# Optimization experiments

Measured on AMD Instinct MI355X. Metric: run time of the kernel, lower is better.

The kernel has to match this reference:

```python
import jax, jax.numpy as jnp
import numpy as np
from jax import lax


def setup_inputs() -> dict:
    key = jax.random.key(0)
    k1, k2, k3, k4, k5 = jax.random.split(key, 5)
    B, Cin, Cout, H, W, K, S = 16, 256, 256, 128, 128, 3, 512
    x = jax.random.normal(k1, (B, Cin, H, W), dtype=jnp.float32)
    style = jax.random.normal(k2, (B, S), dtype=jnp.float32)
    # parameters (kaiming-ish scales)
    conv_w = jax.random.normal(k3, (Cout, Cin, K, K), dtype=jnp.float32) * (1.0 / np.sqrt(Cin * K * K))
    fc_w = jax.random.normal(k4, (Cout, S), dtype=jnp.float32) * (1.0 / np.sqrt(S))
    fc_b = jax.random.normal(k5, (Cout,), dtype=jnp.float32) * 0.01
    return {"x": x, "style": style, "conv_w": conv_w, "fc_w": fc_w, "fc_b": fc_b}


def reference(x, style, conv_w, fc_w, fc_b):
    # style_fc: (B, S) @ (S, Cout) + b -> per-sample per-output-channel scale
    s = style @ fc_w.T + fc_b  # (B, Cout)
    # Modulating W[o] by s[b,o] on the output-channel axis commutes with the
    # convolution, so the per-sample loop is a single conv + channel scale.
    # (Original uses F.conv2d with bias=None, so conv bias is never applied.)
    y = lax.conv_general_dilated(
        x, conv_w,
        window_strides=(1, 1),
        padding=[(1, 1), (1, 1)],
        dimension_numbers=("NCHW", "OIHW", "NCHW"),
    )  # (B, Cout, H, W)
    return y * s[:, :, None, None]
```

## Files before the change

### kernel.cpp

```cpp
#include <hip/hip_runtime.h>
#include <stdint.h>

typedef __attribute__((ext_vector_type(8))) short bf16x8;
typedef __attribute__((ext_vector_type(8))) unsigned short u16x8;
typedef __attribute__((ext_vector_type(4))) float f32x4;

#define NB   16
#define CIN  256
#define COUT 256
#define HH   128
#define WW   128
#define SDIM 512

#define BK 64
#define KPAD 72
#define NCOL 130

#define B_BYTES (3 * NCOL * KPAD * 2)
#define S_BYTES (COUT * 4)
#define LDS_BYTES (B_BYTES + S_BYTES)

__device__ __forceinline__ unsigned short f2bf(float f) {
    unsigned int u = __float_as_uint(f);
    u += 0x7fff + ((u >> 16) & 1);
    return (unsigned short)(u >> 16);
}

__global__ void style_fc_kernel(const float* __restrict__ style,
                                const float* __restrict__ fc_w,
                                const float* __restrict__ fc_b,
                                float* __restrict__ s_out) {
    const int b = blockIdx.x;
    const int co = threadIdx.x;
    const f32x4* st = (const f32x4*)(style + b * SDIM);
    const f32x4* w  = (const f32x4*)(fc_w + co * SDIM);
    float acc = fc_b[co];
    #pragma unroll 4
    for (int k = 0; k < SDIM / 4; ++k) {
        f32x4 a = st[k], c = w[k];
        acc += a.x * c.x + a.y * c.y + a.z * c.z + a.w * c.w;
    }
    s_out[b * COUT + co] = acc;
}

__global__ void wt_transform_kernel(const float* __restrict__ conv_w,
                                    unsigned short* __restrict__ wt) {
    __shared__ unsigned short T[9][256];
    const int co = blockIdx.x;
    const int ci = threadIdx.x;
    const float* src = conv_w + ((size_t)co * CIN + ci) * 9;
    float v[9];
    #pragma unroll
    for (int t = 0; t < 9; ++t) v[t] = src[t];
    #pragma unroll
    for (int t = 0; t < 9; ++t) T[t][ci] = f2bf(v[t]);
    __syncthreads();
    const unsigned int* T32 = (const unsigned int*)&T[0][0];
    unsigned int* out32 = (unsigned int*)wt;
    for (int idx = ci; idx < 1152; idx += 256) {
        const int d = idx & 31;
        const int r = idx >> 5;
        out32[(((size_t)r * COUT + co) << 5) + d] = T32[idx];
    }
}

__global__ void __launch_bounds__(512, 4)
modconv_kernel(const float* __restrict__ x,
               const unsigned short* __restrict__ wt,
               const float* __restrict__ s,
               float* __restrict__ out) {
    extern __shared__ char lds[];
    unsigned short* Bl = (unsigned short*)lds;
    float* Sl = (float*)(lds + B_BYTES);

    const int tid  = threadIdx.x;
    const int lane = tid & 63;
    const int wid  = tid >> 6;
    const int bid  = blockIdx.x;
    const int nid  = (bid & 7) * 256 + (bid >> 3);
    const int bb   = nid >> 7;
    const int h    = nid & 127;

    {
        f32x4 z = {0.f, 0.f, 0.f, 0.f};
        for (int i = tid; i < B_BYTES / 16; i += 512)
            *(f32x4*)(lds + i * 16) = z;
    }
    if (tid < COUT) Sl[tid] = s[bb * COUT + tid];

    f32x4 acc[4][4];
    {
        f32x4 z = {0.f, 0.f, 0.f, 0.f};
        #pragma unroll
        for (int mi = 0; mi < 4; ++mi)
            #pragma unroll
            for (int nj = 0; nj < 4; ++nj)
                acc[mi][nj] = z;
    }

    const int wm = wid >> 1;
    const int wn = wid & 1;
    const int cobase = wm * 64;
    const int wbase  = wn * 64;
    const int l15 = lane & 15;
    const int kl8 = (lane >> 4) * 8;

    __syncthreads();

    #pragma unroll 1
    for (int q = 0; q < 4; ++q) {
        if (q) __syncthreads();
        #pragma unroll
        for (int kh = 0; kh < 3; ++kh) {
            const int r = h + kh - 1;
            if (r >= 0 && r < HH) {
                const float* xs = x + (((size_t)(bb * CIN + q * 64 + wid * 8)) * HH + r) * WW;
                #pragma unroll
                for (int half = 0; half < 2; ++half) {
                    const int w = lane + half * 64;
                    u16x8 vv;
                    #pragma unroll
                    for (int j = 0; j < 8; ++j)
                        vv[j] = f2bf(xs[j * (HH * WW) + w]);
                    *(u16x8*)(Bl + (kh * NCOL + 1 + w) * KPAD + wid * 8) = vv;
                }
            }
        }
        __syncthreads();
        #pragma unroll 3
        for (int t = 0; t < 9; ++t) {
            const int kh = t / 3;
            const int kw = t - kh * 3;
            const unsigned short* wsrc = wt + ((size_t)(t * 4 + q) * COUT + cobase) * 64;
            #pragma unroll
            for (int kkid = 0; kkid < 2; ++kkid) {
                const int kk = kkid * 32;
                bf16x8 a[4], b[4];
                #pragma unroll
                for (int mi = 0; mi < 4; ++mi)
                    a[mi] = *(const bf16x8*)(wsrc + (mi * 16 + l15) * 64 + kk + kl8);
                #pragma unroll
                for (int nj = 0; nj < 4; ++nj)
                    b[nj] = *(const bf16x8*)(Bl + (kh * NCOL + wbase + nj * 16 + l15 + kw) * KPAD + kk + kl8);
                #pragma unroll
                for (int mi = 0; mi < 4; ++mi)
                    #pragma unroll
                    for (int nj = 0; nj < 4; ++nj)
                        acc[mi][nj] = __builtin_amdgcn_mfma_f32_16x16x32_bf16(
                            a[mi], b[nj], acc[mi][nj], 0, 0, 0);
            }
        }
    }

    const int rowD = (lane >> 4) * 4;
    #pragma unroll
    for (int mi = 0; mi < 4; ++mi) {
        #pragma unroll
        for (int r = 0; r < 4; ++r) {
            const int co = cobase + mi * 16 + rowD + r;
            const float sv = Sl[co];
            float* orow = out + (((size_t)(bb * COUT + co) * HH + h) * WW);
            #pragma unroll
            for (int nj = 0; nj < 4; ++nj)
                orow[wbase + nj * 16 + l15] = acc[mi][nj][r] * sv;
        }
    }
}

extern "C" void kernel_launch(void* const* d_in, const int* in_sizes, int n_in,
                              void* d_out, int out_size, void* d_ws, size_t ws_size,
                              hipStream_t stream) {
    const float* x      = (const float*)d_in[0];
    const float* style  = (const float*)d_in[1];
    const float* conv_w = (const float*)d_in[2];
    const float* fc_w   = (const float*)d_in[3];
    const float* fc_b   = (const float*)d_in[4];
    float* out = (float*)d_out;

    float* s_ws = (float*)d_ws;
    unsigned short* wt = (unsigned short*)((char*)d_ws + 16384);

    style_fc_kernel<<<NB, COUT, 0, stream>>>(style, fc_w, fc_b, s_ws);
    wt_transform_kernel<<<COUT, 256, 0, stream>>>(conv_w, wt);
    modconv_kernel<<<NB * HH, 512, LDS_BYTES, stream>>>(x, wt, s_ws, out);
}
```

Baseline: 950.9 us.

## Double-buffer input rows in LDS and prefetch weight fragments across taps

```diff
diff --git a/kernel.cpp b/kernel.cpp
--- a/kernel.cpp
+++ b/kernel.cpp
@@ -12,13 +12,11 @@
 #define WW   128
 #define SDIM 512
 
-#define BK 64
 #define KPAD 72
 #define NCOL 130
-
-#define B_BYTES (3 * NCOL * KPAD * 2)
-#define S_BYTES (COUT * 4)
-#define LDS_BYTES (B_BYTES + S_BYTES)
+#define BHALF (3 * NCOL * KPAD)
+#define B_BYTES (BHALF * 2)
+#define LDS_BYTES (2 * B_BYTES + COUT * 4)
 
 __device__ __forceinline__ unsigned short f2bf(float f) {
     unsigned int u = __float_as_uint(f);
@@ -64,14 +62,15 @@
     }
 }
 
-__global__ void __launch_bounds__(512, 4)
+__global__ void __launch_bounds__(512, 2)
 modconv_kernel(const float* __restrict__ x,
                const unsigned short* __restrict__ wt,
                const float* __restrict__ s,
                float* __restrict__ out) {
     extern __shared__ char lds[];
-    unsigned short* Bl = (unsigned short*)lds;
-    float* Sl = (float*)(lds + B_BYTES);
+    unsigned short* B0 = (unsigned short*)lds;
+    unsigned short* B1 = B0 + BHALF;
+    float* Sl = (float*)(lds + 2 * B_BYTES);
 
     const int tid  = threadIdx.x;
     const int lane = tid & 63;
@@ -83,7 +82,7 @@
 
     {
         f32x4 z = {0.f, 0.f, 0.f, 0.f};
-        for (int i = tid; i < B_BYTES / 16; i += 512)
+        for (int i = tid; i < (2 * B_BYTES) / 16; i += 512)
             *(f32x4*)(lds + i * 16) = z;
     }
     if (tid < COUT) Sl[tid] = s[bb * COUT + tid];
@@ -104,51 +103,95 @@
     const int wbase  = wn * 64;
     const int l15 = lane & 15;
     const int kl8 = (lane >> 4) * 8;
-
-    __syncthreads();
-
-    #pragma unroll 1
-    for (int q = 0; q < 4; ++q) {
-        if (q) __syncthreads();
+    const int g   = wid;
+
+    float xv[3][2][8];
+
+    auto LOADX = [&](int q) {
         #pragma unroll
         for (int kh = 0; kh < 3; ++kh) {
             const int r = h + kh - 1;
             if (r >= 0 && r < HH) {
-                const float* xs = x + (((size_t)(bb * CIN + q * 64 + wid * 8)) * HH + r) * WW;
-                #pragma unroll
-                for (int half = 0; half < 2; ++half) {
-                    const int w = lane + half * 64;
-                    u16x8 vv;
+                const float* xs = x + (((size_t)(bb * CIN + q * 64 + g * 8)) * HH + r) * WW;
+                #pragma unroll
+                for (int half = 0; half < 2; ++half)
                     #pragma unroll
                     for (int j = 0; j < 8; ++j)
-                        vv[j] = f2bf(xs[j * (HH * WW) + w]);
-                    *(u16x8*)(Bl + (kh * NCOL + 1 + w) * KPAD + wid * 8) = vv;
-                }
+                        xv[kh][half][j] = xs[j * (HH * WW) + lane + half * 64];
+            } else {
+                #pragma unroll
+                for (int half = 0; half < 2; ++half)
+                    #pragma unroll
+                    for (int j = 0; j < 8; ++j)
+                        xv[kh][half][j] = 0.0f;
             }
         }
-        __syncthreads();
-        #pragma unroll 3
+    };
+    auto WRITEX = [&](unsigned short* Bd) {
+        #pragma unroll
+        for (int kh = 0; kh < 3; ++kh)
+            #pragma unroll
+            for (int half = 0; half < 2; ++half) {
+                u16x8 vv;
+                #pragma unroll
+                for (int j = 0; j < 8; ++j) vv[j] = f2bf(xv[kh][half][j]);
+                *(u16x8*)(Bd + (kh * NCOL + 1 + lane + half * 64) * KPAD + g * 8) = vv;
+            }
+    };
+    auto LOADA = [&](bf16x8* a, int q, int t, int kk) {
+        const unsigned short* p = wt + (((size_t)(t * 4 + q) * COUT + cobase + l15) << 6) + kk + kl8;
+        #pragma unroll
+        for (int mi = 0; mi < 4; ++mi)
+            a[mi] = *(const bf16x8*)(p + (mi << 10));
+    };
+    auto LOADB = [&](bf16x8* b, const unsigned short* Bc, int kh, int kw, int kk) {
+        #pragma unroll
+        for (int nj = 0; nj < 4; ++nj)
+            b[nj] = *(const bf16x8*)(Bc + (kh * NCOL + wbase + nj * 16 + l15 + kw) * KPAD + kk + kl8);
+    };
+
+    __syncthreads();
+    LOADX(0);
+    WRITEX(B0);
+    __syncthreads();
+
+    bf16x8 aA[4], aB[4];
+    LOADA(aA, 0, 0, 0);
+
+    #pragma unroll 1
+    for (int q = 0; q < 4; ++q) {
+        unsigned short* Bc = (q & 1) ? B1 : B0;
+        unsigned short* Bn = (q & 1) ? B0 : B1;
+        if (q < 3) LOADX(q + 1);
+        const int qn = (q < 3) ? q + 1 : 3;
+
+        #pragma unroll
         for (int t = 0; t < 9; ++t) {
             const int kh = t / 3;
             const int kw = t - kh * 3;
-            const unsigned short* wsrc = wt + ((size_t)(t * 4 + q) * COUT + cobase) * 64;
-            #pragma unroll
-            for (int kkid = 0; kkid < 2; ++kkid) {
-                const int kk = kkid * 32;
-                bf16x8 a[4], b[4];
-                #pragma unroll
-                for (int mi = 0; mi < 4; ++mi)
-                    a[mi] = *(const bf16x8*)(wsrc + (mi * 16 + l15) * 64 + kk + kl8);
+            bf16x8 b[4];
+            LOADB(b, Bc, kh, kw, 0);
+            LOADA(aB, q, t, 32);
+            #pragma unroll
+            for (int mi = 0; mi < 4; ++mi)
                 #pragma unroll
                 for (int nj = 0; nj < 4; ++nj)
-                    b[nj] = *(const bf16x8*)(Bl + (kh * NCOL + wbase + nj * 16 + l15 + kw) * KPAD + kk + kl8);
-                #pragma unroll
-                for (int mi = 0; mi < 4; ++mi)
-                    #pragma unroll
-                    for (int nj = 0; nj < 4; ++nj)
-                        acc[mi][nj] = __builtin_amdgcn_mfma_f32_16x16x32_bf16(
-                            a[mi], b[nj], acc[mi][nj], 0, 0, 0);
-            }
+                    acc[mi][nj] = __builtin_amdgcn_mfma_f32_16x16x32_bf16(
+                        aA[mi], b[nj], acc[mi][nj], 0, 0, 0);
+            LOADB(b, Bc, kh, kw, 32);
+            if (t < 8) LOADA(aA, q, t + 1, 0);
+            else       LOADA(aA, qn, 0, 0);
+            #pragma unroll
+            for (int mi = 0; mi < 4; ++mi)
+                #pragma unroll
+                for (int nj = 0; nj < 4; ++nj)
+                    acc[mi][nj] = __builtin_amdgcn_mfma_f32_16x16x32_bf16(
+                        aB[mi], b[nj], acc[mi][nj], 0, 0, 0);
+        }
+
+        if (q < 3) {
+            WRITEX(Bn);
+            __syncthreads();
         }
     }
 
@@ -180,6 +223,9 @@
     float* s_ws = (float*)d_ws;
     unsigned short* wt = (unsigned short*)((char*)d_ws + 16384);
 
+    hipFuncSetAttribute(reinterpret_cast<const void*>(modconv_kernel),
+                        hipFuncAttributeMaxDynamicSharedMemorySize, LDS_BYTES);
+
     style_fc_kernel<<<NB, COUT, 0, stream>>>(style, fc_w, fc_b, s_ws);
     wt_transform_kernel<<<COUT, 256, 0, stream>>>(conv_w, wt);
     modconv_kernel<<<NB * HH, 512, LDS_BYTES, stream>>>(x, wt, s_ws, out);
```

Measured after the change: 956.4 us. Within noise of the previous version (+0.6%).
